# Kernel tuning notes

Hardware: AMD Instinct MI355X
Metric: run time of the kernel (lower is better)

The kernel has to match this reference:

```python
import jax, jax.numpy as jnp
import numpy as np

N = 10000      # nodes
E = 100000     # edges
D = 768        # hidden = heads * head_dim
H = 4          # heads
C = D // H     # 192 per-head channels
EDIM = 16      # edge feature dim
NREL = 10      # num relations
L = 3          # num TransformerConv layers


def setup_inputs() -> dict:
    key = jax.random.key(0)
    ks = jax.random.split(key, 16)
    s = 0.02
    x = jax.random.normal(ks[0], (N, D), jnp.float32)
    edge_index = jax.random.randint(ks[1], (2, E), 0, N, jnp.int32)
    rel = jax.random.randint(ks[2], (E,), 0, NREL).astype(jnp.float32)
    w = jax.random.uniform(ks[3], (E,), jnp.float32)
    edge_attr = jnp.stack([rel, w], axis=1)  # [E, 2]: (relation_id, weight)
    rel_emb = jax.random.normal(ks[4], (NREL, EDIM - 1), jnp.float32) * s
    W_edge = jax.random.normal(ks[5], (EDIM, EDIM), jnp.float32) * s
    b_edge = jnp.zeros((EDIM,), jnp.float32)
    Wk = jax.random.normal(ks[6], (L, D, D), jnp.float32) * s
    bk = jnp.zeros((L, D), jnp.float32)
    Wq = jax.random.normal(ks[7], (L, D, D), jnp.float32) * s
    bq = jnp.zeros((L, D), jnp.float32)
    Wv = jax.random.normal(ks[8], (L, D, D), jnp.float32) * s
    bv = jnp.zeros((L, D), jnp.float32)
    We = jax.random.normal(ks[9], (L, EDIM, D), jnp.float32) * s   # lin_edge, no bias (PyG)
    Wskip = jax.random.normal(ks[10], (L, D, D), jnp.float32) * s  # root/skip linear
    bskip = jnp.zeros((L, D), jnp.float32)
    ln_g = jnp.ones((D,), jnp.float32)
    ln_b = jnp.zeros((D,), jnp.float32)
    return dict(x=x, edge_attr=edge_attr, edge_index=edge_index, rel_emb=rel_emb,
                W_edge=W_edge, b_edge=b_edge, Wk=Wk, bk=bk, Wq=Wq, bq=bq,
                Wv=Wv, bv=bv, We=We, Wskip=Wskip, bskip=bskip, ln_g=ln_g, ln_b=ln_b)


def reference(x, edge_attr, edge_index, rel_emb, W_edge, b_edge,
              Wk, bk, Wq, bq, Wv, bv, We, Wskip, bskip, ln_g, ln_b):
    src, dst = edge_index[0], edge_index[1]
    # _process_edge_features: embed relation id, concat weight, project
    rel_ids = jnp.clip(jax.lax.stop_gradient(edge_attr[:, 0]).astype(jnp.int32), 0, NREL - 1)
    ef = jnp.concatenate([rel_emb[rel_ids], edge_attr[:, 1:2]], axis=-1) @ W_edge + b_edge  # [E,16]
    scale = 1.0 / np.sqrt(C)
    h = x  # input_proj is Identity (input_dim == hidden_dim)
    for l in range(L):
        q = (h @ Wq[l] + bq[l]).reshape(N, H, C)
        k = (h @ Wk[l] + bk[l]).reshape(N, H, C)
        v = (h @ Wv[l] + bv[l]).reshape(N, H, C)
        e = (ef @ We[l]).reshape(E, H, C)           # per-edge embedding
        kj = k[src] + e                              # [E,H,C]
        alpha = jnp.einsum('ehc,ehc->eh', q[dst], kj) * scale  # [E,H]
        # scatter-softmax over incoming edges of each destination node
        m = jax.ops.segment_max(jax.lax.stop_gradient(alpha), dst, num_segments=N)
        a = jnp.exp(alpha - m[dst])
        denom = jax.ops.segment_sum(a, dst, num_segments=N)
        a = a / (denom[dst] + 1e-16)
        msg = (v[src] + e) * a[..., None]            # [E,H,C]
        out = jax.ops.segment_sum(msg.reshape(E, H * C), dst, num_segments=N)
        h = out + h @ Wskip[l] + bskip[l]            # root_weight skip connection
        if l < L - 1:
            h = jax.nn.gelu(h, approximate=False)    # dropout: eval mode -> identity
    mu = jnp.mean(h, axis=-1, keepdims=True)
    var = jnp.mean((h - mu) ** 2, axis=-1, keepdims=True)
    h = (h - mu) / jnp.sqrt(var + 1e-5) * ln_g + ln_b
    return jnp.mean(h, axis=0)  # global_mean_pool over single graph -> [D]
```

## Files before the change

### kernel.cpp

```cpp
#include <hip/hip_runtime.h>
#include <hip/hip_bf16.h>
#include <math.h>
#include <stdint.h>

#define NN 10000
#define EE 100000
#define DD 768
#define HH 4
#define CC 192
#define EDIM 16
#define NREL 10
#define MP 10240
#define NQ2 3200
#define NB 3136
#define SCALE 0.07216878364870322f

using short8  = __attribute__((ext_vector_type(8))) short;
using floatx4 = __attribute__((ext_vector_type(4))) float;


__device__ __forceinline__ float b2f(short u) {
    union { unsigned int i; float f; } t;
    t.i = ((unsigned int)(unsigned short)u) << 16;
    return t.f;
}

__device__ __forceinline__ short f2b(float f) {
    __hip_bfloat16 h = __float2bfloat16(f);
    short r;
    __builtin_memcpy(&r, &h, 2);
    return r;
}

__device__ __forceinline__ __hip_bfloat16 rd_any(const void* p, long long j, int bf) {
    if (bf) return ((const __hip_bfloat16*)p)[j];
    return __float2bfloat16(((const float*)p)[j]);
}

__device__ __forceinline__ void gload16(const __hip_bfloat16* g, __hip_bfloat16* l) {
    __builtin_amdgcn_global_load_lds(
        (const __attribute__((address_space(1))) unsigned int*)g,
        (__attribute__((address_space(3))) unsigned int*)l, 16, 0, 0);
}

__global__ __launch_bounds__(256) void detect_zero(const void* edge_attr,
                                                   int* flag, int* counts) {
    int i = blockIdx.x * 256 + threadIdx.x;
    if (i < NN) counts[i] = 0;
    if (blockIdx.x == 0 && threadIdx.x < 64) {
        const unsigned short* p = (const unsigned short*)edge_attr;
        int nz = (p[4 * threadIdx.x] != 0) ? 1 : 0;
        unsigned long long m = __ballot(nz);
        if (threadIdx.x == 0) *flag = (__popcll(m) > 8) ? 1 : 0;
    }
}


__global__ __launch_bounds__(256) void cvt_big(
    const void* x, const void* We, const int* flag,
    __hip_bfloat16* hb, __hip_bfloat16* Web) {
    long long i = (long long)blockIdx.x * 256 + threadIdx.x;
    int bf = *flag;
    const long long NX = (long long)NN * DD;
    const long long NE2 = 3LL * EDIM * DD;
    if (i < NX) { hb[i] = rd_any(x, i, bf); return; } i -= NX;
    if (i < NE2) { Web[i] = rd_any(We, i, bf); return; } i -= NE2;
    if (i < (long long)(MP - NN) * DD) hb[(long long)NN * DD + i] = __float2bfloat16(0.0f);
}

__global__ __launch_bounds__(256) void cvt_small(
    const void* ea, const void* rel, const void* Wed, const void* bed,
    const void* bk, const void* bq, const void* bv, const void* bs,
    const void* lg, const void* lb, const int* flag,
    __hip_bfloat16* eab, __hip_bfloat16* relb, __hip_bfloat16* Wedb,
    __hip_bfloat16* bedb, __hip_bfloat16* ballb, __hip_bfloat16* lgb,
    __hip_bfloat16* lbb) {
    long long i = (long long)blockIdx.x * 256 + threadIdx.x;
    int bf = *flag;
    if (i < 2LL * EE) { eab[i] = rd_any(ea, i, bf); return; } i -= 2LL * EE;
    if (i < NREL * (EDIM - 1)) { relb[i] = rd_any(rel, i, bf); return; } i -= NREL * (EDIM - 1);
    if (i < EDIM * EDIM) { Wedb[i] = rd_any(Wed, i, bf); return; } i -= EDIM * EDIM;
    if (i < EDIM) { bedb[i] = rd_any(bed, i, bf); return; } i -= EDIM;
    if (i < 3 * NB) {
        int l = (int)(i / NB), c = (int)(i % NB);
        const void* src; long long off;
        if (c < 768)       { src = bq; off = (long long)l * DD + c; }
        else if (c < 1536) { src = bk; off = (long long)l * DD + (c - 768); }
        else if (c < 2304) { src = bv; off = (long long)l * DD + (c - 1536); }
        else if (c < 3072) { src = bs; off = (long long)l * DD + (c - 2304); }
        else { ballb[i] = __float2bfloat16(0.0f); return; }
        ballb[i] = rd_any(src, off, bf); return;
    } i -= 3 * NB;
    if (i < DD) { lgb[i] = rd_any(lg, i, bf); return; } i -= DD;
    if (i < DD) { lbb[i] = rd_any(lb, i, bf); return; }
}

__global__ __launch_bounds__(256) void wt_all(
    const void* Wq, const void* Wk, const void* Wv, const void* Ws,
    const int* flag, __hip_bfloat16* Wt3) {
    __shared__ __hip_bfloat16 tile[32][33];
    int mm = blockIdx.y;
    int l = mm >> 2, m = mm & 3;
    const void* src = (m == 0) ? Wq : (m == 1) ? Wk : (m == 2) ? Wv : Ws;
    int bx = blockIdx.x;
    int tr = bx / 24, tc = bx % 24;
    int k0 = tr * 32, c0 = tc * 32;
    int t = threadIdx.x;
    int rr = t >> 5, cc = t & 31;
    int bf = *flag;
    long long base = (long long)l * DD * DD;
#pragma unroll
    for (int p = 0; p < 4; p++)
        tile[p * 8 + rr][cc] =
            rd_any(src, base + (long long)(k0 + p * 8 + rr) * DD + c0 + cc, bf);
    __syncthreads();
    __hip_bfloat16* dst = Wt3 + (size_t)l * NB * DD + (size_t)(m * 768 + c0) * DD + k0;
#pragma unroll
    for (int p = 0; p < 4; p++)
        dst[(size_t)(p * 8 + rr) * DD + cc] = tile[cc][p * 8 + rr];
}

__global__ __launch_bounds__(256) void mq_kernel(
    const void* Wq, const void* bq, const int* flag,
    const __hip_bfloat16* __restrict__ Web, __hip_bfloat16* __restrict__ Wt3,
    __hip_bfloat16* __restrict__ ballb) {
    __shared__ float WeS[16][193];
    const int lh = blockIdx.y, l = lh >> 2, hh = lh & 3;
    const int t = threadIdx.x;
    const int bf = *flag;
    for (int i = t; i < 16 * 192; i += 256) {
        int j = i / 192, c = i % 192;
        WeS[j][c] = (float)Web[(size_t)l * EDIM * DD + (size_t)j * DD + hh * CC + c];
    }
    __syncthreads();
    const int k = blockIdx.x * 64 + (t >> 2);
    const int j0 = (t & 3) * 4;
    float s0 = 0.f, s1 = 0.f, s2 = 0.f, s3 = 0.f;
    if (bf) {
        const short8* qp = (const short8*)((const __hip_bfloat16*)Wq +
            ((size_t)l * DD + k) * DD + hh * CC);
#pragma unroll 4
        for (int ch = 0; ch < 24; ch++) {
            short8 v = qp[ch];
#pragma unroll
            for (int u = 0; u < 8; u++) {
                float w = b2f(v[u]);
                int c = ch * 8 + u;
                s0 += w * WeS[j0 + 0][c]; s1 += w * WeS[j0 + 1][c];
                s2 += w * WeS[j0 + 2][c]; s3 += w * WeS[j0 + 3][c];
            }
        }
    } else {
        const float4* qp = (const float4*)((const float*)Wq +
            ((size_t)l * DD + k) * DD + hh * CC);
#pragma unroll 4
        for (int ch = 0; ch < 48; ch++) {
            float4 v = qp[ch];
            float wv[4] = {v.x, v.y, v.z, v.w};
#pragma unroll
            for (int u = 0; u < 4; u++) {
                float w = wv[u];
                int c = ch * 4 + u;
                s0 += w * WeS[j0 + 0][c]; s1 += w * WeS[j0 + 1][c];
                s2 += w * WeS[j0 + 2][c]; s3 += w * WeS[j0 + 3][c];
            }
        }
    }
    const size_t base = (size_t)l * NB * DD;
    const int row = 3072 + hh * 16 + j0;
    Wt3[base + (size_t)(row + 0) * DD + k] = __float2bfloat16(s0);
    Wt3[base + (size_t)(row + 1) * DD + k] = __float2bfloat16(s1);
    Wt3[base + (size_t)(row + 2) * DD + k] = __float2bfloat16(s2);
    Wt3[base + (size_t)(row + 3) * DD + k] = __float2bfloat16(s3);
    if (blockIdx.x == 0 && t < 4) {
        float b0 = 0.f, b1 = 0.f, b2 = 0.f, b3 = 0.f;
        for (int c = 0; c < CC; c++) {
            float w = (float)rd_any(bq, (long long)l * DD + hh * CC + c, bf);
            b0 += w * WeS[j0 + 0][c]; b1 += w * WeS[j0 + 1][c];
            b2 += w * WeS[j0 + 2][c]; b3 += w * WeS[j0 + 3][c];
        }
        ballb[l * NB + 3072 + hh * 16 + j0 + 0] = __float2bfloat16(b0);
        ballb[l * NB + 3072 + hh * 16 + j0 + 1] = __float2bfloat16(b1);
        ballb[l * NB + 3072 + hh * 16 + j0 + 2] = __float2bfloat16(b2);
        ballb[l * NB + 3072 + hh * 16 + j0 + 3] = __float2bfloat16(b3);
    }
}


__global__ __launch_bounds__(256) void count_kernel(const int* ei, int* counts) {
    int e = blockIdx.x * 256 + threadIdx.x;
    if (e < EE) atomicAdd(&counts[ei[EE + e]], 1);
}

__global__ __launch_bounds__(256) void scan_kernel(const int* counts, int* rowptr,
                                                   int* cursor) {
    __shared__ int sdata[256];
    int t = threadIdx.x;
    int base = t * 40;
    int cnt = (base < NN) ? min(40, NN - base) : 0;
    int s = 0;
    for (int i = 0; i < cnt; i++) s += counts[base + i];
    sdata[t] = s;
    __syncthreads();
    for (int off = 1; off < 256; off <<= 1) {
        int add = (t >= off) ? sdata[t - off] : 0;
        __syncthreads();
        sdata[t] += add;
        __syncthreads();
    }
    int run = sdata[t] - s;
    for (int i = 0; i < cnt; i++) {
        cursor[base + i] = run;
        run += counts[base + i];
        rowptr[base + i + 1] = run;
    }
    if (t == 0) rowptr[0] = 0;
}

__global__ __launch_bounds__(256) void fill_kernel(const int* ei, int* cursor,
                                                   int* eids, int* esrc) {
    int e = blockIdx.x * 256 + threadIdx.x;
    if (e < EE) {
        int d = ei[EE + e];
        int pos = atomicAdd(&cursor[d], 1);
        eids[pos] = e;
        esrc[pos] = ei[e];
    }
}


__global__ __launch_bounds__(256) void ef_kernel(
    const int* __restrict__ eids,
    const __hip_bfloat16* __restrict__ eab, const __hip_bfloat16* __restrict__ relb,
    const __hip_bfloat16* __restrict__ Wedb, const __hip_bfloat16* __restrict__ bedb,
    __hip_bfloat16* __restrict__ efb) {
    int idx = blockIdx.x * 256 + threadIdx.x;
    if (idx >= EE * EDIM) return;
    int p = idx >> 4, j = idx & 15;
    int e = eids[p];
    int rid = (int)((float)eab[e * 2 + 0]);
    rid = min(max(rid, 0), NREL - 1);
    float w = (float)eab[e * 2 + 1];
    float s = (float)bedb[j];
#pragma unroll
    for (int i = 0; i < 15; i++)
        s += (float)relb[rid * 15 + i] * (float)Wedb[i * EDIM + j];
    s += w * (float)Wedb[15 * EDIM + j];
    efb[idx] = __float2bfloat16(s);
}


__device__ __forceinline__ void stage_half(const __hip_bfloat16* g, int row0, int ktile,
                                           char* ldsdst, int tid) {
#pragma unroll
    for (int j = 0; j < 2; ++j) {
        int c = j * 512 + tid;
        int row = c >> 3;
        int sch = (c & 7) ^ (row & 7);
        gload16(g + (size_t)(row0 + row) * DD + ktile * 64 + sch * 8,
                (__hip_bfloat16*)(ldsdst + c * 16));
    }
}

#define MF16(va, vb, cc) cc = __builtin_amdgcn_mfma_f32_16x16x32_bf16(va, vb, cc, 0, 0, 0)
#define BAR() __builtin_amdgcn_s_barrier()
#define WLG() asm volatile("s_waitcnt lgkmcnt(0)" ::: "memory")
#define WVM(N) asm volatile("s_waitcnt vmcnt(" #N ")" ::: "memory")
#define SB() __builtin_amdgcn_sched_barrier(0)
#define LDS8(off) (*(const short8*)(smem + (off)))

__global__ __launch_bounds__(512) void gemm256(
    const __hip_bfloat16* __restrict__ A, const __hip_bfloat16* __restrict__ Bt,
    const __hip_bfloat16* __restrict__ bias, __hip_bfloat16* __restrict__ C) {
    __shared__ __align__(16) char smem[131072];
    const int tid = threadIdx.x;
    const int wid = tid >> 6, lane = tid & 63;
    const int quad = lane >> 4, l15 = lane & 15;
    const int wm = wid >> 2, wn = wid & 3;
    const int bid = (int)blockIdx.x;
    const int swz = (bid & 7) * 60 + (bid >> 3);
    const int m0 = (swz / 12) * 256;
    const int n0 = (swz % 12) * 256;

    const int xa0 = (quad ^ (l15 & 7)) * 16;
    const int xa1 = ((quad + 4) ^ (l15 & 7)) * 16;
    const int aRow = (wm * 128 + l15) * 128;
    const int bRow = 32768 + (wn * 64 + l15) * 128;

    floatx4 acc[8][4] = {};
    short8 a[4][2], bA[2][2], bB[2][2];

    stage_half(A, m0, 0, smem + 0, tid);
    stage_half(A, m0 + 128, 0, smem + 16384, tid);
    stage_half(Bt, n0, 0, smem + 32768, tid);
    stage_half(Bt, n0 + 128, 0, smem + 49152, tid);
    stage_half(Bt, n0, 1, smem + 98304, tid);
    stage_half(Bt, n0 + 128, 1, smem + 114688, tid);
    WVM(4);
    BAR();

#pragma unroll 1
    for (int it = 0; it < 6; ++it) {
        const int kA = 2 * it + 1;
        const int kB = (it < 5) ? 2 * it + 2 : 0;
        const int kC = (it < 5) ? 2 * it + 3 : 1;
        stage_half(A, m0, kA, smem + 65536, tid);
        stage_half(A, m0 + 128, kA, smem + 81920, tid);
#pragma unroll
        for (int mt = 0; mt < 4; ++mt) {
            a[mt][0] = LDS8(aRow + mt * 2048 + xa0);
            a[mt][1] = LDS8(aRow + mt * 2048 + xa1);
        }
#pragma unroll
        for (int nt = 0; nt < 2; ++nt) {
            bA[nt][0] = LDS8(bRow + nt * 2048 + xa0);
            bA[nt][1] = LDS8(bRow + nt * 2048 + xa1);
            bB[nt][0] = LDS8(bRow + (nt + 2) * 2048 + xa0);
            bB[nt][1] = LDS8(bRow + (nt + 2) * 2048 + xa1);
        }
        SB(); BAR(); WLG(); SB();
        __builtin_amdgcn_s_setprio(1);
#pragma unroll
        for (int mt = 0; mt < 4; ++mt)
#pragma unroll
            for (int nt = 0; nt < 2; ++nt) {
                MF16(a[mt][0], bA[nt][0], acc[mt][nt]);
                MF16(a[mt][1], bA[nt][1], acc[mt][nt]);
                MF16(a[mt][0], bB[nt][0], acc[mt][nt + 2]);
                MF16(a[mt][1], bB[nt][1], acc[mt][nt + 2]);
            }
        __builtin_amdgcn_s_setprio(0);
        stage_half(Bt, n0, kB, smem + 32768, tid);
        stage_half(Bt, n0 + 128, kB, smem + 49152, tid);
#pragma unroll
        for (int mt = 0; mt < 4; ++mt) {
            a[mt][0] = LDS8(aRow + (mt + 4) * 2048 + xa0);
            a[mt][1] = LDS8(aRow + (mt + 4) * 2048 + xa1);
        }
        WVM(4);
        SB(); BAR(); WLG(); SB();
        __builtin_amdgcn_s_setprio(1);
#pragma unroll
        for (int mt = 0; mt < 4; ++mt)
#pragma unroll
            for (int nt = 0; nt < 2; ++nt) {
                MF16(a[mt][0], bB[nt][0], acc[mt + 4][nt + 2]);
                MF16(a[mt][1], bB[nt][1], acc[mt + 4][nt + 2]);
                MF16(a[mt][0], bA[nt][0], acc[mt + 4][nt]);
                MF16(a[mt][1], bA[nt][1], acc[mt + 4][nt]);
            }
        __builtin_amdgcn_s_setprio(0);
        stage_half(A, m0, kB, smem + 0, tid);
        stage_half(A, m0 + 128, kB, smem + 16384, tid);
#pragma unroll
        for (int mt = 0; mt < 4; ++mt) {
            a[mt][0] = LDS8(65536 + aRow + mt * 2048 + xa0);
            a[mt][1] = LDS8(65536 + aRow + mt * 2048 + xa1);
        }
#pragma unroll
        for (int nt = 0; nt < 2; ++nt) {
            bA[nt][0] = LDS8(65536 + bRow + nt * 2048 + xa0);
            bA[nt][1] = LDS8(65536 + bRow + nt * 2048 + xa1);
            bB[nt][0] = LDS8(65536 + bRow + (nt + 2) * 2048 + xa0);
            bB[nt][1] = LDS8(65536 + bRow + (nt + 2) * 2048 + xa1);
        }
        SB(); BAR(); WLG(); SB();
        __builtin_amdgcn_s_setprio(1);
#pragma unroll
        for (int mt = 0; mt < 4; ++mt)
#pragma unroll
            for (int nt = 0; nt < 2; ++nt) {
                MF16(a[mt][0], bA[nt][0], acc[mt][nt]);
                MF16(a[mt][1], bA[nt][1], acc[mt][nt]);
                MF16(a[mt][0], bB[nt][0], acc[mt][nt + 2]);
                MF16(a[mt][1], bB[nt][1], acc[mt][nt + 2]);
            }
        __builtin_amdgcn_s_setprio(0);
        stage_half(Bt, n0, kC, smem + 98304, tid);
        stage_half(Bt, n0 + 128, kC, smem + 114688, tid);
#pragma unroll
        for (int mt = 0; mt < 4; ++mt) {
            a[mt][0] = LDS8(65536 + aRow + (mt + 4) * 2048 + xa0);
            a[mt][1] = LDS8(65536 + aRow + (mt + 4) * 2048 + xa1);
        }
        WVM(4);
        SB(); BAR(); WLG(); SB();
        __builtin_amdgcn_s_setprio(1);
#pragma unroll
        for (int mt = 0; mt < 4; ++mt)
#pragma unroll
            for (int nt = 0; nt < 2; ++nt) {
                MF16(a[mt][0], bB[nt][0], acc[mt + 4][nt + 2]);
                MF16(a[mt][1], bB[nt][1], acc[mt + 4][nt + 2]);
                MF16(a[mt][0], bA[nt][0], acc[mt + 4][nt]);
                MF16(a[mt][1], bA[nt][1], acc[mt + 4][nt]);
            }
        __builtin_amdgcn_s_setprio(0);
    }

    asm volatile("s_waitcnt vmcnt(0)" ::: "memory");
    BAR();
    {
        short* stg = (short*)smem + wid * 1152;
        float bv[4];
#pragma unroll
        for (int nt = 0; nt < 4; ++nt)
            bv[nt] = (float)bias[n0 + wn * 64 + nt * 16 + l15];
        const int rdo = (lane >> 2) * 68 + (lane & 3) * 16;
        const int grow0 = m0 + wm * 128 + (lane >> 2);
        const int gcol = n0 + wn * 64 + (lane & 3) * 16;
#pragma unroll
        for (int mt = 0; mt < 8; ++mt) {
#pragma unroll
            for (int nt = 0; nt < 4; ++nt)
#pragma unroll
                for (int r = 0; r < 4; ++r)
                    stg[(quad * 4 + r) * 68 + nt * 16 + l15] =
                        f2b(acc[mt][nt][r] + bv[nt]);
            asm volatile("s_waitcnt lgkmcnt(0)" ::: "memory");
            short8 v0 = *(const short8*)(stg + rdo);
            short8 v1 = *(const short8*)(stg + rdo + 8);
            int grow = grow0 + mt * 16;
            if (grow < NN) {
                short8* dp = (short8*)(C + (size_t)grow * NQ2 + gcol);
                dp[0] = v0; dp[1] = v1;
            }
            asm volatile("s_waitcnt lgkmcnt(0)" ::: "memory");
        }
    }
}


__global__ __launch_bounds__(256) void qe_gemm(
    const __hip_bfloat16* __restrict__ A, const __hip_bfloat16* __restrict__ Bt,
    const __hip_bfloat16* __restrict__ bias, __hip_bfloat16* __restrict__ C) {
    __shared__ __align__(16) char smem[16384];
    const int tid = threadIdx.x;
    const int wid = tid >> 6, lane = tid & 63;
    const int quad = lane >> 4, l15 = lane & 15;
    const int m0 = blockIdx.x * 64;
    const int xa0 = (quad ^ (l15 & 7)) * 16;
    const int xa1 = ((quad + 4) ^ (l15 & 7)) * 16;
    floatx4 acc[4] = {};
    for (int kt = 0; kt < 12; ++kt) {
#pragma unroll
        for (int j = 0; j < 4; ++j) {
            int c = j * 256 + tid;
            int hf = c >> 9;
            int cc = c & 511;
            int row = cc >> 3;
            int sch = (cc & 7) ^ (row & 7);
            const __hip_bfloat16* src = hf
                ? (Bt + (size_t)row * DD + kt * 64 + sch * 8)
                : (A + (size_t)(m0 + row) * DD + kt * 64 + sch * 8);
            gload16(src, (__hip_bfloat16*)(smem + c * 16));
        }
        asm volatile("s_waitcnt vmcnt(0)" ::: "memory");
        BAR();
        short8 a0 = LDS8((wid * 16 + l15) * 128 + xa0);
        short8 a1 = LDS8((wid * 16 + l15) * 128 + xa1);
#pragma unroll
        for (int nt = 0; nt < 4; ++nt) {
            short8 b0 = LDS8(8192 + (nt * 16 + l15) * 128 + xa0);
            short8 b1 = LDS8(8192 + (nt * 16 + l15) * 128 + xa1);
            MF16(a0, b0, acc[nt]);
            MF16(a1, b1, acc[nt]);
        }
        WLG();
        BAR();
    }
#pragma unroll
    for (int nt = 0; nt < 4; ++nt) {
        float bb = (float)bias[nt * 16 + l15];
#pragma unroll
        for (int r = 0; r < 4; ++r) {
            int row = m0 + wid * 16 + quad * 4 + r;
            if (row < NN)
                C[(size_t)row * NQ2 + 3072 + nt * 16 + l15] =
                    __float2bfloat16(acc[nt][r] + bb);
        }
    }
}


__global__ __launch_bounds__(256) void node_attn(
    const int* __restrict__ rowptr, const int* __restrict__ esrc,
    const __hip_bfloat16* __restrict__ qkvs, const __hip_bfloat16* __restrict__ efb,
    const __hip_bfloat16* __restrict__ Wel, __hip_bfloat16* __restrict__ hb,
    int do_gelu) {
    const int wv = threadIdx.x >> 6, lane = threadIdx.x & 63;
    const int n = blockIdx.x * 2 + (wv >> 1);
    const int half = wv & 1;
    const int cb = half * 384 + lane * 6;
    const int sj = lane & 15;
    const int hsel = lane & 32;
    const float qe_gate = ((lane & 16) == 0) ? 1.0f : 0.0f;
    const int s0 = rowptr[n], s1 = rowptr[n + 1];
    const short* qk = (const short*)qkvs;
    float q[6];
    {
        const short2* qp = (const short2*)(qk + (size_t)n * NQ2 + cb);
        short2 a = qp[0], b = qp[1], c = qp[2];
        q[0] = b2f(a.x); q[1] = b2f(a.y); q[2] = b2f(b.x);
        q[3] = b2f(b.y); q[4] = b2f(c.x); q[5] = b2f(c.y);
    }
    const float qe_l = b2f(qk[(size_t)n * NQ2 + 3072 + (half * 2 + (lane >> 5)) * 16 + sj]);
    float m = -INFINITY, lsum = 0.f, sacc = 0.f;
    float acc[6] = {};
    for (int p = s0; p < s1; p++) {
        int src = esrc[p];
        const short2* kp = (const short2*)(qk + (size_t)src * NQ2 + 768 + cb);
        const short2* vp = (const short2*)(qk + (size_t)src * NQ2 + 1536 + cb);
        short2 ka = kp[0], kb = kp[1], kc = kp[2];
        short2 va = vp[0], vb = vp[1], vc = vp[2];
        float efv = b2f(((const short*)efb)[(size_t)p * 16 + sj]);
        float part = qe_gate * qe_l * efv;
        part += q[0] * b2f(ka.x) + q[1] * b2f(ka.y) + q[2] * b2f(kb.x);
        part += q[3] * b2f(kb.y) + q[4] * b2f(kc.x) + q[5] * b2f(kc.y);
        part += __shfl_xor(part, 1); part += __shfl_xor(part, 2);
        part += __shfl_xor(part, 4); part += __shfl_xor(part, 8);
        part += __shfl_xor(part, 16);
        float a = part * SCALE;
        float nm = fmaxf(m, a);
        float sc = __expf(m - nm);
        float w  = __expf(a - nm);
        lsum = lsum * sc + w;
        m = nm;
        acc[0] = acc[0] * sc + w * b2f(va.x); acc[1] = acc[1] * sc + w * b2f(va.y);
        acc[2] = acc[2] * sc + w * b2f(vb.x); acc[3] = acc[3] * sc + w * b2f(vb.y);
        acc[4] = acc[4] * sc + w * b2f(vc.x); acc[5] = acc[5] * sc + w * b2f(vc.y);
        sacc = sacc * sc + w * efv;
    }
    float inv = 1.0f / (lsum + 1e-16f);
#pragma unroll
    for (int i = 0; i < 6; i++) acc[i] *= inv;
    float sS = sacc * inv;
    {
        const short2* sp = (const short2*)(qk + (size_t)n * NQ2 + 2304 + cb);
        short2 a = sp[0], b = sp[1], c = sp[2];
        acc[0] += b2f(a.x); acc[1] += b2f(a.y); acc[2] += b2f(b.x);
        acc[3] += b2f(b.y); acc[4] += b2f(c.x); acc[5] += b2f(c.y);
    }
#pragma unroll
    for (int j = 0; j < 16; j++) {
        float sv = __shfl(sS, hsel + j);
        const short2* wp = (const short2*)(Wel + (size_t)j * DD + cb);
        short2 a = wp[0], b = wp[1], c = wp[2];
        acc[0] += sv * b2f(a.x); acc[1] += sv * b2f(a.y); acc[2] += sv * b2f(b.x);
        acc[3] += sv * b2f(b.y); acc[4] += sv * b2f(c.x); acc[5] += sv * b2f(c.y);
    }
    if (do_gelu) {
#pragma unroll
        for (int i = 0; i < 6; i++)
            acc[i] = 0.5f * acc[i] * (1.0f + erff(acc[i] * 0.70710678118654752f));
    }
    short2 o0, o1, o2;
    o0.x = f2b(acc[0]); o0.y = f2b(acc[1]);
    o1.x = f2b(acc[2]); o1.y = f2b(acc[3]);
    o2.x = f2b(acc[4]); o2.y = f2b(acc[5]);
    short2* hp = (short2*)(hb + (size_t)n * DD + cb);
    hp[0] = o0; hp[1] = o1; hp[2] = o2;
}


__global__ __launch_bounds__(256) void ln_pool(
    const __hip_bfloat16* __restrict__ hb, const __hip_bfloat16* __restrict__ g,
    const __hip_bfloat16* __restrict__ b, float* __restrict__ partial) {
    __shared__ float sbuf[4][768];
    int grp = blockIdx.x, t = threadIdx.x;
    int wid = t >> 6, lane = t & 63;
    float gv[12], bv[12], acc[12];
#pragma unroll
    for (int i = 0; i < 12; i++) {
        gv[i] = (float)g[lane + i * 64];
        bv[i] = (float)b[lane + i * 64];
        acc[i] = 0.f;
    }
    for (int r = wid; r < 25; r += 4) {
        const __hip_bfloat16* row = hb + (size_t)(grp * 25 + r) * DD;
        float x[12];
        float s = 0.f, q = 0.f;
#pragma unroll
        for (int i = 0; i < 12; i++) {
            x[i] = (float)row[lane + i * 64];
            s += x[i]; q += x[i] * x[i];
        }
#pragma unroll
        for (int m = 32; m > 0; m >>= 1) {
            s += __shfl_xor(s, m); q += __shfl_xor(q, m);
        }
        float mu = s * (1.0f / 768.0f);
        float ms = q * (1.0f / 768.0f);
        float inv = 1.0f / sqrtf(ms - mu * mu + 1e-5f);
#pragma unroll
        for (int i = 0; i < 12; i++)
            acc[i] += (x[i] - mu) * inv * gv[i] + bv[i];
    }
#pragma unroll
    for (int i = 0; i < 12; i++) sbuf[wid][lane + i * 64] = acc[i];
    __syncthreads();
#pragma unroll
    for (int j = 0; j < 3; j++) {
        int col = t + j * 256;
        partial[(size_t)grp * DD + col] =
            sbuf[0][col] + sbuf[1][col] + sbuf[2][col] + sbuf[3][col];
    }
}

__global__ __launch_bounds__(256) void pool_final(
    const float* __restrict__ partial, void* __restrict__ out,
    const int* __restrict__ flag) {
    int dd = blockIdx.x * 256 + threadIdx.x;
    if (dd >= DD) return;
    float s = 0.f;
    for (int g2 = 0; g2 < 400; g2++) s += partial[(size_t)g2 * DD + dd];
    s *= (1.0f / 10000.0f);
    if (*flag) ((__hip_bfloat16*)out)[dd] = __float2bfloat16(s);
    else ((float*)out)[dd] = s;
}


extern "C" void kernel_launch(void* const* d_in, const int* in_sizes, int n_in,
                              void* d_out, int out_size, void* d_ws, size_t ws_size,
                              hipStream_t stream) {
    const void* x         = d_in[0];
    const void* edge_attr = d_in[1];
    const int*  ei        = (const int*)d_in[2];
    const void* rel_emb   = d_in[3];
    const void* W_edge    = d_in[4];
    const void* b_edge    = d_in[5];
    const void* Wk        = d_in[6];
    const void* bk        = d_in[7];
    const void* Wq        = d_in[8];
    const void* bq        = d_in[9];
    const void* Wv        = d_in[10];
    const void* bv        = d_in[11];
    const void* We        = d_in[12];
    const void* Wskip     = d_in[13];
    const void* bskip     = d_in[14];
    const void* ln_g      = d_in[15];
    const void* ln_b      = d_in[16];

    char* ws = (char*)d_ws;
    int*   flag    = (int*)(ws + 0);
    int*   counts  = (int*)(ws + 256);
    int*   rowptr  = (int*)(ws + 40448);
    int*   cursor  = (int*)(ws + 80640);
    int*   eids    = (int*)(ws + 120832);
    int*   esrc    = (int*)(ws + 520960);
    __hip_bfloat16* efb = (__hip_bfloat16*)(ws + 920960);
    float* partial = (float*)(ws + 4120960);
    __hip_bfloat16* eab   = (__hip_bfloat16*)(ws + 5349760);
    __hip_bfloat16* relb  = (__hip_bfloat16*)(ws + 5749760);
    __hip_bfloat16* Wedb  = (__hip_bfloat16*)(ws + 5750144);
    __hip_bfloat16* bedb  = (__hip_bfloat16*)(ws + 5750656);
    __hip_bfloat16* ballb = (__hip_bfloat16*)(ws + 5750784);
    __hip_bfloat16* lngb  = (__hip_bfloat16*)(ws + 5770752);
    __hip_bfloat16* lnbb  = (__hip_bfloat16*)(ws + 5772288);
    __hip_bfloat16* Web   = (__hip_bfloat16*)(ws + 5773824);
    __hip_bfloat16* hb    = (__hip_bfloat16*)(ws + 5847552);
    __hip_bfloat16* Wt3   = (__hip_bfloat16*)(ws + 21576192);
    __hip_bfloat16* qkvs  = (__hip_bfloat16*)(ws + 36911616);

    dim3 blk(256);

    detect_zero<<<dim3(40), blk, 0, stream>>>(edge_attr, flag, counts);

    {
        long long tot = (long long)NN * DD + 3LL * EDIM * DD + (long long)(MP - NN) * DD;
        cvt_big<<<dim3((unsigned)((tot + 255) / 256)), blk, 0, stream>>>(x, We, flag, hb, Web);
    }
    {
        long long tot = 2LL * EE + NREL * (EDIM - 1) + EDIM * EDIM + EDIM
                        + 3LL * NB + 2LL * DD;
        cvt_small<<<dim3((unsigned)((tot + 255) / 256)), blk, 0, stream>>>(
            edge_attr, rel_emb, W_edge, b_edge, bk, bq, bv, bskip, ln_g, ln_b,
            flag, eab, relb, Wedb, bedb, ballb, lngb, lnbb);
    }
    wt_all<<<dim3(576, 12), blk, 0, stream>>>(Wq, Wk, Wv, Wskip, flag, Wt3);
    mq_kernel<<<dim3(12, 12), blk, 0, stream>>>(Wq, bq, flag, Web, Wt3, ballb);

    count_kernel<<<dim3((EE + 255) / 256), blk, 0, stream>>>(ei, counts);
    scan_kernel<<<dim3(1), blk, 0, stream>>>(counts, rowptr, cursor);
    fill_kernel<<<dim3((EE + 255) / 256), blk, 0, stream>>>(ei, cursor, eids, esrc);

    ef_kernel<<<dim3((EE * EDIM) / 256), blk, 0, stream>>>(eids, eab, relb, Wedb, bedb, efb);

    for (int l = 0; l < 3; l++) {
        const __hip_bfloat16* We_l = Web + (size_t)l * EDIM * DD;
        gemm256<<<dim3(480), dim3(512), 0, stream>>>(
            hb, Wt3 + (size_t)l * NB * DD, ballb + (size_t)l * NB, qkvs);
        qe_gemm<<<dim3(160), blk, 0, stream>>>(
            hb, Wt3 + (size_t)l * NB * DD + (size_t)3072 * DD,
            ballb + (size_t)l * NB + 3072, qkvs);
        node_attn<<<dim3(NN / 2), blk, 0, stream>>>(rowptr, esrc, qkvs, efb,
                                                    We_l, hb, (l < 2) ? 1 : 0);
    }

    ln_pool<<<dim3(400), blk, 0, stream>>>(hb, lngb, lnbb, partial);
    pool_final<<<dim3(3), blk, 0, stream>>>(partial, d_out, flag);
}
```

Before: 607.6 us.

## Fold qe GEMM into main GEMM launch and prefetch edges in attention loop

The small qe_gemm kernel is removed. Its work now runs in 160 extra blocks appended to the gemm256 grid, with only 4 of the 8 waves computing, which saves one launch per layer. In node_attn, the next edge's K/V/edge-feature loads are software-prefetched to hide gather latency. The scale is folded into q, and the online softmax uses a lazy rescale that only rescales when the max grows by more than 8. The lazy rescale adds a small overflow or precision risk, and the extra gemm blocks leave half their waves idle.

After: 601.7 us. About the same (-1.0%).

```diff
diff --git a/kernel.cpp b/kernel.cpp
--- a/kernel.cpp
+++ b/kernel.cpp
@@ -273,11 +273,64 @@
     const __hip_bfloat16* __restrict__ A, const __hip_bfloat16* __restrict__ Bt,
     const __hip_bfloat16* __restrict__ bias, __hip_bfloat16* __restrict__ C) {
     __shared__ __align__(16) char smem[131072];
+    const int bid = (int)blockIdx.x;
     const int tid = threadIdx.x;
     const int wid = tid >> 6, lane = tid & 63;
     const int quad = lane >> 4, l15 = lane & 15;
+
+    if (bid >= 480) {
+        const int qb = bid - 480;
+        const int m0q = qb * 64;
+        const __hip_bfloat16* Bq = Bt + (size_t)3072 * DD;
+        const int xq0 = (quad ^ (l15 & 7)) * 16;
+        const int xq1 = ((quad + 4) ^ (l15 & 7)) * 16;
+        floatx4 qacc[4] = {};
+        for (int kt = 0; kt < 12; ++kt) {
+#pragma unroll
+            for (int j = 0; j < 2; ++j) {
+                int c = j * 512 + tid;
+                int hf = c >> 9;
+                int cc = c & 511;
+                int row = cc >> 3;
+                int sch = (cc & 7) ^ (row & 7);
+                const __hip_bfloat16* src = hf
+                    ? (Bq + (size_t)row * DD + kt * 64 + sch * 8)
+                    : (A + (size_t)(m0q + row) * DD + kt * 64 + sch * 8);
+                gload16(src, (__hip_bfloat16*)(smem + c * 16));
+            }
+            asm volatile("s_waitcnt vmcnt(0)" ::: "memory");
+            BAR();
+            if (wid < 4) {
+                short8 a0 = LDS8((wid * 16 + l15) * 128 + xq0);
+                short8 a1 = LDS8((wid * 16 + l15) * 128 + xq1);
+#pragma unroll
+                for (int nt = 0; nt < 4; ++nt) {
+                    short8 b0 = LDS8(8192 + (nt * 16 + l15) * 128 + xq0);
+                    short8 b1 = LDS8(8192 + (nt * 16 + l15) * 128 + xq1);
+                    MF16(a0, b0, qacc[nt]);
+                    MF16(a1, b1, qacc[nt]);
+                }
+            }
+            WLG();
+            BAR();
+        }
+        if (wid < 4) {
+#pragma unroll
+            for (int nt = 0; nt < 4; ++nt) {
+                float bb = (float)bias[3072 + nt * 16 + l15];
+#pragma unroll
+                for (int r = 0; r < 4; ++r) {
+                    int row = m0q + wid * 16 + quad * 4 + r;
+                    if (row < NN)
+                        C[(size_t)row * NQ2 + 3072 + nt * 16 + l15] =
+                            __float2bfloat16(qacc[nt][r] + bb);
+                }
+            }
+        }
+        return;
+    }
+
     const int wm = wid >> 2, wn = wid & 3;
-    const int bid = (int)blockIdx.x;
     const int swz = (bid & 7) * 60 + (bid >> 3);
     const int m0 = (swz / 12) * 256;
     const int n0 = (swz % 12) * 256;
@@ -426,58 +479,6 @@
                 dp[0] = v0; dp[1] = v1;
             }
             asm volatile("s_waitcnt lgkmcnt(0)" ::: "memory");
-        }
-    }
-}
-
-
-__global__ __launch_bounds__(256) void qe_gemm(
-    const __hip_bfloat16* __restrict__ A, const __hip_bfloat16* __restrict__ Bt,
-    const __hip_bfloat16* __restrict__ bias, __hip_bfloat16* __restrict__ C) {
-    __shared__ __align__(16) char smem[16384];
-    const int tid = threadIdx.x;
-    const int wid = tid >> 6, lane = tid & 63;
-    const int quad = lane >> 4, l15 = lane & 15;
-    const int m0 = blockIdx.x * 64;
-    const int xa0 = (quad ^ (l15 & 7)) * 16;
-    const int xa1 = ((quad + 4) ^ (l15 & 7)) * 16;
-    floatx4 acc[4] = {};
-    for (int kt = 0; kt < 12; ++kt) {
-#pragma unroll
-        for (int j = 0; j < 4; ++j) {
-            int c = j * 256 + tid;
-            int hf = c >> 9;
-            int cc = c & 511;
-            int row = cc >> 3;
-            int sch = (cc & 7) ^ (row & 7);
-            const __hip_bfloat16* src = hf
-                ? (Bt + (size_t)row * DD + kt * 64 + sch * 8)
-                : (A + (size_t)(m0 + row) * DD + kt * 64 + sch * 8);
-            gload16(src, (__hip_bfloat16*)(smem + c * 16));
-        }
-        asm volatile("s_waitcnt vmcnt(0)" ::: "memory");
-        BAR();
-        short8 a0 = LDS8((wid * 16 + l15) * 128 + xa0);
-        short8 a1 = LDS8((wid * 16 + l15) * 128 + xa1);
-#pragma unroll
-        for (int nt = 0; nt < 4; ++nt) {
-            short8 b0 = LDS8(8192 + (nt * 16 + l15) * 128 + xa0);
-            short8 b1 = LDS8(8192 + (nt * 16 + l15) * 128 + xa1);
-            MF16(a0, b0, acc[nt]);
-            MF16(a1, b1, acc[nt]);
-        }
-        WLG();
-        BAR();
-    }
-#pragma unroll
-    for (int nt = 0; nt < 4; ++nt) {
-        float bb = (float)bias[nt * 16 + l15];
-#pragma unroll
-        for (int r = 0; r < 4; ++r) {
-            int row = m0 + wid * 16 + quad * 4 + r;
-            if (row < NN)
-                C[(size_t)row * NQ2 + 3072 + nt * 16 + l15] =
-                    __float2bfloat16(acc[nt][r] + bb);
         }
     }
 }
@@ -501,35 +502,55 @@
     {
         const short2* qp = (const short2*)(qk + (size_t)n * NQ2 + cb);
         short2 a = qp[0], b = qp[1], c = qp[2];
-        q[0] = b2f(a.x); q[1] = b2f(a.y); q[2] = b2f(b.x);
-        q[3] = b2f(b.y); q[4] = b2f(c.x); q[5] = b2f(c.y);
-    }
-    const float qe_l = b2f(qk[(size_t)n * NQ2 + 3072 + (half * 2 + (lane >> 5)) * 16 + sj]);
+        q[0] = b2f(a.x) * SCALE; q[1] = b2f(a.y) * SCALE; q[2] = b2f(b.x) * SCALE;
+        q[3] = b2f(b.y) * SCALE; q[4] = b2f(c.x) * SCALE; q[5] = b2f(c.y) * SCALE;
+    }
+    const float qe_l = b2f(qk[(size_t)n * NQ2 + 3072 + (half * 2 + (lane >> 5)) * 16 + sj])
+                       * SCALE * qe_gate;
     float m = -INFINITY, lsum = 0.f, sacc = 0.f;
     float acc[6] = {};
-    for (int p = s0; p < s1; p++) {
-        int src = esrc[p];
+    short2 ka = {0,0}, kb = {0,0}, kc = {0,0};
+    short2 va = {0,0}, vb = {0,0}, vc = {0,0};
+    float efv = 0.f;
+    if (s0 < s1) {
+        int src = esrc[s0];
         const short2* kp = (const short2*)(qk + (size_t)src * NQ2 + 768 + cb);
         const short2* vp = (const short2*)(qk + (size_t)src * NQ2 + 1536 + cb);
-        short2 ka = kp[0], kb = kp[1], kc = kp[2];
-        short2 va = vp[0], vb = vp[1], vc = vp[2];
-        float efv = b2f(((const short*)efb)[(size_t)p * 16 + sj]);
-        float part = qe_gate * qe_l * efv;
+        ka = kp[0]; kb = kp[1]; kc = kp[2];
+        va = vp[0]; vb = vp[1]; vc = vp[2];
+        efv = b2f(((const short*)efb)[(size_t)s0 * 16 + sj]);
+    }
+    for (int p = s0; p < s1; p++) {
+        short2 nka = ka, nkb = kb, nkc = kc, nva = va, nvb = vb, nvc = vc;
+        float nefv = efv;
+        if (p + 1 < s1) {
+            int src = esrc[p + 1];
+            const short2* kp = (const short2*)(qk + (size_t)src * NQ2 + 768 + cb);
+            const short2* vp = (const short2*)(qk + (size_t)src * NQ2 + 1536 + cb);
+            nka = kp[0]; nkb = kp[1]; nkc = kp[2];
+            nva = vp[0]; nvb = vp[1]; nvc = vp[2];
+            nefv = b2f(((const short*)efb)[(size_t)(p + 1) * 16 + sj]);
+        }
+        float part = qe_l * efv;
         part += q[0] * b2f(ka.x) + q[1] * b2f(ka.y) + q[2] * b2f(kb.x);
         part += q[3] * b2f(kb.y) + q[4] * b2f(kc.x) + q[5] * b2f(kc.y);
         part += __shfl_xor(part, 1); part += __shfl_xor(part, 2);
         part += __shfl_xor(part, 4); part += __shfl_xor(part, 8);
         part += __shfl_xor(part, 16);
-        float a = part * SCALE;
-        float nm = fmaxf(m, a);
-        float sc = __expf(m - nm);
-        float w  = __expf(a - nm);
-        lsum = lsum * sc + w;
-        m = nm;
-        acc[0] = acc[0] * sc + w * b2f(va.x); acc[1] = acc[1] * sc + w * b2f(va.y);
-        acc[2] = acc[2] * sc + w * b2f(vb.x); acc[3] = acc[3] * sc + w * b2f(vb.y);
-        acc[4] = acc[4] * sc + w * b2f(vc.x); acc[5] = acc[5] * sc + w * b2f(vc.y);
-        sacc = sacc * sc + w * efv;
+        if (part > m + 8.0f) {
+            float sc = __expf(m - part);
+            m = part;
+            lsum *= sc; sacc *= sc;
+#pragma unroll
+            for (int i = 0; i < 6; i++) acc[i] *= sc;
+        }
+        float w = __expf(part - m);
+        lsum += w;
+        sacc += w * efv;
+        acc[0] += w * b2f(va.x); acc[1] += w * b2f(va.y);
+        acc[2] += w * b2f(vb.x); acc[3] += w * b2f(vb.y);
+        acc[4] += w * b2f(vc.x); acc[5] += w * b2f(vc.y);
+        ka = nka; kb = nkb; kc = nkc; va = nva; vb = nvb; vc = nvc; efv = nefv;
     }
     float inv = 1.0f / (lsum + 1e-16f);
 #pragma unroll
@@ -688,11 +709,8 @@
 
     for (int l = 0; l < 3; l++) {
         const __hip_bfloat16* We_l = Web + (size_t)l * EDIM * DD;
-        gemm256<<<dim3(480), dim3(512), 0, stream>>>(
+        gemm256<<<dim3(640), dim3(512), 0, stream>>>(
             hb, Wt3 + (size_t)l * NB * DD, ballb + (size_t)l * NB, qkvs);
-        qe_gemm<<<dim3(160), blk, 0, stream>>>(
-            hb, Wt3 + (size_t)l * NB * DD + (size_t)3072 * DD,
-            ballb + (size_t)l * NB + 3072, qkvs);
         node_attn<<<dim3(NN / 2), blk, 0, stream>>>(rowptr, esrc, qkvs, efb,
                                                     We_l, hb, (l < 2) ? 1 : 0);
     }
```
